# Performance work log

Measured on AMD Instinct MI355X. Metric: run time of the kernel, lower is better.

The kernel has to match this reference:

```python
import jax, jax.numpy as jnp
import numpy as np

NEG_INF = -1e9


def setup_inputs() -> dict:
    key = jax.random.key(0)
    k1, k2, k3 = jax.random.split(key, 3)
    B, C, Q, D = 64, 1024, 128, 128
    context = jax.random.normal(k1, (B, C, D), dtype=jnp.float32)
    query = jax.random.normal(k2, (B, Q, D), dtype=jnp.float32)
    W = jax.random.normal(k3, (3 * D, 1), dtype=jnp.float32)
    query_mask = jnp.ones((B, Q), dtype=jnp.float32)
    return {"context": context, "query": query, "W": W, "query_mask": query_mask}


def reference(context, query, W, query_mask):
    # Dense(1) over concat([c, q, c*q]) decomposes as c.w_c + q.w_q + (c*w_s).q
    D = context.shape[-1]
    w = W[:, 0]
    w_c, w_q, w_s = w[:D], w[D:2 * D], w[2 * D:]
    c_term = jnp.einsum('bcd,d->bc', context, w_c)          # [B,C]
    q_term = jnp.einsum('bqd,d->bq', query, w_q)            # [B,Q]
    s_term = jnp.einsum('bcd,bqd->bcq', context * w_s, query)  # [B,C,Q]
    S = c_term[:, :, None] + q_term[:, None, :] + s_term    # [B,C,Q]
    S = S + (1.0 - query_mask)[:, None, :] * NEG_INF
    c2q_scores = jax.nn.softmax(S, axis=2)                  # [B,C,Q]
    c2q = jnp.einsum('bcq,bqd->bcd', c2q_scores, query)     # [B,C,D]
    q2c_scores = jax.nn.softmax(jnp.max(S, axis=2), axis=1)  # [B,C]
    q2c = jnp.einsum('bc,bcd->bd', q2c_scores, context)     # [B,D]
    q2c = q2c[:, None, :]                                   # broadcast over C
    out = jnp.concatenate([context, c2q, context * c2q, context * q2c], axis=-1)
    return out
```

## Files before the change

### kernel.cpp

```cpp
#include <hip/hip_runtime.h>

#define NEGINF -1000000000.0f

typedef __attribute__((ext_vector_type(4))) float f32x4;
typedef _Float16 half8 __attribute__((ext_vector_type(8)));
typedef _Float16 half4 __attribute__((ext_vector_type(4)));

constexpr int Bn = 64, Cn = 1024, Qn = 128, Dn = 128;
constexpr int QSTR = 144;
constexpr int CSTR = 132;


__global__ __launch_bounds__(256) void k1_kernel(
    const float* __restrict__ ctx, const float* __restrict__ qry,
    const float* __restrict__ W, const float* __restrict__ mask,
    float* __restrict__ out, float* __restrict__ ws_part, float* __restrict__ ws_ms)
{
    __shared__ char smem[77376];
    _Float16* qrow = (_Float16*)smem;
    _Float16* qT2  = (_Float16*)(smem + 36864);
    float* wfull = (float*)(smem + 73728);
    float* qts   = (float*)(smem + 75264);
    float* cts   = (float*)(smem + 75776);
    float* mloc  = (float*)(smem + 76288);
    float* wv    = (float*)(smem + 76800);
    float* red   = (float*)(smem + 77312);
    float* partf = (float*)(smem + 36864);
    float* cq    = (float*)smem;

    const int b = blockIdx.y, cg = blockIdx.x, c0 = cg * 128;
    const int t = threadIdx.x;
    const float* ctxB = ctx + (size_t)b * Cn * Dn;
    const float* qryB = qry + (size_t)b * Qn * Dn;

    for (int i = t; i < 384; i += 256) wfull[i] = W[i];
    __syncthreads();

    {
        int q = t >> 1, h = t & 1;
        const float* qr = qryB + q * Dn + h * 64;
        int p = ((q >> 5) << 5) + 8 * ((q >> 2) & 3) + (q & 3) + 4 * ((q >> 4) & 1);
        float acc = 0.f;
        for (int j = 0; j < 64; j += 4) {
            f32x4 v = *(const f32x4*)(qr + j);
            int d = h * 64 + j;
            acc += v.x * wfull[128 + d] + v.y * wfull[128 + d + 1]
                 + v.z * wfull[128 + d + 2] + v.w * wfull[128 + d + 3];
            half4 hv;
            hv[0] = (_Float16)v.x; hv[1] = (_Float16)v.y;
            hv[2] = (_Float16)v.z; hv[3] = (_Float16)v.w;
            *(half4*)&qrow[q * QSTR + d] = hv;
            qT2[(d + 0) * QSTR + p] = hv[0];
            qT2[(d + 1) * QSTR + p] = hv[1];
            qT2[(d + 2) * QSTR + p] = hv[2];
            qT2[(d + 3) * QSTR + p] = hv[3];
        }
        acc += __shfl_xor(acc, 1);
        if (h == 0) qts[q] = acc + (1.0f - mask[b * Qn + q]) * NEGINF;
    }
    {
        int c = t >> 1, h = t & 1;
        const float* cr = ctxB + (size_t)(c0 + c) * Dn + h * 64;
        float acc = 0.f;
        for (int j = 0; j < 64; j += 4) {
            f32x4 v = *(const f32x4*)(cr + j);
            int d = h * 64 + j;
            acc += v.x * wfull[d] + v.y * wfull[d + 1] + v.z * wfull[d + 2] + v.w * wfull[d + 3];
        }
        acc += __shfl_xor(acc, 1);
        if (h == 0) cts[c] = acc;
    }
    __syncthreads();

    const int wave = t >> 6, lane = t & 63, g = lane >> 4, l15 = lane & 15;
    const int cw = wave * 32;

    f32x4 acc1[8][2] = {};
#pragma unroll
    for (int kk = 0; kk < 4; ++kk) {
        const int dbase = kk * 32 + g * 8;
        f32x4 w0 = *(const f32x4*)&wfull[256 + dbase];
        f32x4 w1 = *(const f32x4*)&wfull[256 + dbase + 4];
        half8 ah[2], al[2];
#pragma unroll
        for (int nt = 0; nt < 2; ++nt) {
            const float* p = ctxB + (size_t)(c0 + cw + nt * 16 + l15) * Dn + dbase;
            f32x4 v0 = *(const f32x4*)p, v1 = *(const f32x4*)(p + 4);
            float av[8] = {v0.x * w0.x, v0.y * w0.y, v0.z * w0.z, v0.w * w0.w,
                           v1.x * w1.x, v1.y * w1.y, v1.z * w1.z, v1.w * w1.w};
#pragma unroll
            for (int j = 0; j < 8; ++j) {
                _Float16 hh = (_Float16)av[j];
                ah[nt][j] = hh;
                al[nt][j] = (_Float16)(av[j] - (float)hh);
            }
        }
#pragma unroll
        for (int mt = 0; mt < 8; ++mt) {
            half8 qf = *(const half8*)&qrow[(mt * 16 + l15) * QSTR + dbase];
#pragma unroll
            for (int nt = 0; nt < 2; ++nt) {
                acc1[mt][nt] = __builtin_amdgcn_mfma_f32_16x16x32_f16(qf, ah[nt], acc1[mt][nt], 0, 0, 0);
                acc1[mt][nt] = __builtin_amdgcn_mfma_f32_16x16x32_f16(qf, al[nt], acc1[mt][nt], 0, 0, 0);
            }
        }
    }

#pragma unroll
    for (int mt = 0; mt < 8; ++mt)
#pragma unroll
        for (int r = 0; r < 4; ++r) {
            float qv = qts[mt * 16 + g * 4 + r];
            acc1[mt][0][r] += qv;
            acc1[mt][1][r] += qv;
        }

    float psum[2];
#pragma unroll
    for (int nt = 0; nt < 2; ++nt) {
        float mx = -3.4e38f;
#pragma unroll
        for (int mt = 0; mt < 8; ++mt)
#pragma unroll
            for (int r = 0; r < 4; ++r) mx = fmaxf(mx, acc1[mt][nt][r]);
        mx = fmaxf(mx, __shfl_xor(mx, 16));
        mx = fmaxf(mx, __shfl_xor(mx, 32));
        float sum = 0.f;
#pragma unroll
        for (int mt = 0; mt < 8; ++mt)
#pragma unroll
            for (int r = 0; r < 4; ++r) {
                float pv = __expf(acc1[mt][nt][r] - mx);
                acc1[mt][nt][r] = pv;
                sum += pv;
            }
        sum += __shfl_xor(sum, 16);
        sum += __shfl_xor(sum, 32);
        psum[nt] = sum;
        int cl = cw + nt * 16 + l15;
        if (g == 0) mloc[cl] = mx + cts[cl];
    }

    half8 pa[4][2];
#pragma unroll
    for (int kk2 = 0; kk2 < 4; ++kk2)
#pragma unroll
        for (int nt = 0; nt < 2; ++nt)
#pragma unroll
            for (int j = 0; j < 8; ++j)
                pa[kk2][nt][j] = (_Float16)acc1[2 * kk2 + (j >> 2)][nt][j & 3];

    float inv[2][4];
#pragma unroll
    for (int nt = 0; nt < 2; ++nt)
#pragma unroll
        for (int r = 0; r < 4; ++r)
            inv[nt][r] = 1.0f / __shfl(psum[nt], g * 4 + r);

    f32x4 acc2[2][8] = {};
#pragma unroll
    for (int kk2 = 0; kk2 < 4; ++kk2)
#pragma unroll
        for (int ntD = 0; ntD < 8; ++ntD) {
            half8 qb = *(const half8*)&qT2[(ntD * 16 + l15) * QSTR + kk2 * 32 + 8 * g];
#pragma unroll
            for (int nt1 = 0; nt1 < 2; ++nt1)
                acc2[nt1][ntD] = __builtin_amdgcn_mfma_f32_16x16x32_f16(pa[kk2][nt1], qb, acc2[nt1][ntD], 0, 0, 0);
        }
    __syncthreads();

    float Mloc;
    {
        float v = (t < 128) ? mloc[t] : -3.4e38f;
        float m = v;
#pragma unroll
        for (int off = 1; off < 64; off <<= 1) m = fmaxf(m, __shfl_xor(m, off));
        if (lane == 0) red[wave] = m;
        __syncthreads();
        Mloc = fmaxf(fmaxf(red[0], red[1]), fmaxf(red[2], red[3]));
        float e = (t < 128) ? __expf(v - Mloc) : 0.f;
        if (t < 128) wv[t] = e;
        float s = e;
#pragma unroll
        for (int off = 1; off < 64; off <<= 1) s += __shfl_xor(s, off);
        if (lane == 0) red[4 + wave] = s;
        __syncthreads();
    }
    float Sloc = red[4] + red[5] + red[6] + red[7];
    {
        int grp = t >> 5, d4 = (t & 31) * 4;
        const float* cb = ctxB + (size_t)(c0 + grp * 16) * Dn;
        f32x4 a = {};
        for (int i = 0; i < 16; ++i) {
            f32x4 cv = *(const f32x4*)(cb + (size_t)i * Dn + d4);
            float w = wv[grp * 16 + i];
            a.x += w * cv.x; a.y += w * cv.y; a.z += w * cv.z; a.w += w * cv.w;
        }
        *(f32x4*)&partf[grp * 128 + d4] = a;
        __syncthreads();
        if (t < 128) {
            float s = 0.f;
#pragma unroll
            for (int g2 = 0; g2 < 8; ++g2) s += partf[g2 * 128 + t];
            ws_part[((size_t)(b * 8 + cg)) * 128 + t] = s;
        }
        if (t == 0) {
            ws_ms[(b * 8 + cg) * 2 + 0] = Mloc;
            ws_ms[(b * 8 + cg) * 2 + 1] = Sloc;
        }
    }
    __syncthreads();

#pragma unroll
    for (int nt1 = 0; nt1 < 2; ++nt1)
#pragma unroll
        for (int r = 0; r < 4; ++r) {
            int c = cw + nt1 * 16 + g * 4 + r;
            float is = inv[nt1][r];
#pragma unroll
            for (int ntD = 0; ntD < 8; ++ntD)
                cq[c * CSTR + ntD * 16 + l15] = acc2[nt1][ntD][r] * is;
        }
    __syncthreads();
    for (int step = 0; step < 16; ++step) {
        int c = (t >> 5) + step * 8, d4 = (t & 31) * 4;
        f32x4 q = *(const f32x4*)&cq[c * CSTR + d4];
        f32x4 cv = *(const f32x4*)(ctxB + (size_t)(c0 + c) * Dn + d4);
        float* orow = out + ((size_t)(b * Cn + c0 + c)) * 512;
        *(f32x4*)(orow + 128 + d4) = q;
        f32x4 pr;
        pr.x = cv.x * q.x; pr.y = cv.y * q.y; pr.z = cv.z * q.z; pr.w = cv.w * q.w;
        *(f32x4*)(orow + 256 + d4) = pr;
    }
}

__global__ __launch_bounds__(256) void k3_kernel(
    const float* __restrict__ ctx, const float* __restrict__ ws_part,
    const float* __restrict__ ws_ms, float* __restrict__ out)
{
    __shared__ float q2cs[128];
    const int ct = blockIdx.x, b = blockIdx.y, t = threadIdx.x;
    if (t < 128) {
        const float* ms = ws_ms + b * 16;
        float Mg = -3.4e38f;
#pragma unroll
        for (int i = 0; i < 8; ++i) Mg = fmaxf(Mg, ms[2 * i]);
        float num = 0.f, den = 0.f;
#pragma unroll
        for (int i = 0; i < 8; ++i) {
            float e = __expf(ms[2 * i] - Mg);
            num += e * ws_part[((size_t)(b * 8 + i)) * 128 + t];
            den += e * ms[2 * i + 1];
        }
        q2cs[t] = num / den;
    }
    __syncthreads();
    const float* cb = ctx + ((size_t)b * Cn + ct * 128) * Dn;
    float* ob = out + ((size_t)(b * Cn) + ct * 128) * 512;
    for (int step = 0; step < 16; ++step) {
        int c = (t >> 5) + step * 8, d4 = (t & 31) * 4;
        f32x4 v = *(const f32x4*)(cb + (size_t)c * Dn + d4);
        f32x4 q = *(const f32x4*)&q2cs[d4];
        *(f32x4*)(ob + (size_t)c * 512 + d4) = v;
        f32x4 w;
        w.x = v.x * q.x; w.y = v.y * q.y; w.z = v.z * q.z; w.w = v.w * q.w;
        *(f32x4*)(ob + (size_t)c * 512 + 384 + d4) = w;
    }
}

extern "C" void kernel_launch(void* const* d_in, const int* in_sizes, int n_in,
                              void* d_out, int out_size, void* d_ws, size_t ws_size,
                              hipStream_t stream) {
    const float* ctx  = (const float*)d_in[0];
    const float* qry  = (const float*)d_in[1];
    const float* W    = (const float*)d_in[2];
    const float* mask = (const float*)d_in[3];
    float* out = (float*)d_out;

    float* ws_part = (float*)d_ws;
    float* ws_ms   = ws_part + (size_t)Bn * 8 * 128;

    k1_kernel<<<dim3(8, Bn), 256, 0, stream>>>(ctx, qry, W, mask, out, ws_part, ws_ms);
    k3_kernel<<<dim3(8, Bn), 256, 0, stream>>>(ctx, ws_part, ws_ms, out);
}
```

Baseline: 55.71 us.

## Fuse q2c pass into main kernel with per-batch atomic grid sync

Merges the second kernel into the first: each block publishes its partial q2c sums with atomic stores, bumps a per-batch counter, then spin-waits until all eight blocks of its batch have arrived before computing q2c and writing all four output slices. Context rows are kept in registers so they are not read from global memory again. A small reset kernel zeroes the counters, shared memory is shrunk (QSTR reduced) and launch bounds request two blocks per CU so that co-residency makes the spin-wait safe. The risks are deadlock if the blocks of one batch are not co-resident, higher register pressure from the cached context rows, and a serialized wait on the slowest block.

Measured after the change: 104.9 us. 88.3% more time.

```diff
diff --git a/kernel.cpp b/kernel.cpp
--- a/kernel.cpp
+++ b/kernel.cpp
@@ -7,25 +7,31 @@
 typedef _Float16 half4 __attribute__((ext_vector_type(4)));
 
 constexpr int Bn = 64, Cn = 1024, Qn = 128, Dn = 128;
-constexpr int QSTR = 144;
+constexpr int QSTR = 136;
 constexpr int CSTR = 132;
 
 
-__global__ __launch_bounds__(256) void k1_kernel(
+__global__ void reset_kernel(unsigned* __restrict__ cnt) {
+    cnt[threadIdx.x] = 0u;
+}
+
+__global__ __launch_bounds__(256, 2) void fused_kernel(
     const float* __restrict__ ctx, const float* __restrict__ qry,
     const float* __restrict__ W, const float* __restrict__ mask,
-    float* __restrict__ out, float* __restrict__ ws_part, float* __restrict__ ws_ms)
+    float* __restrict__ out, float* __restrict__ ws_part,
+    float* __restrict__ ws_ms, unsigned* __restrict__ cnt)
 {
-    __shared__ char smem[77376];
+    __shared__ char smem[73792];
     _Float16* qrow = (_Float16*)smem;
-    _Float16* qT2  = (_Float16*)(smem + 36864);
-    float* wfull = (float*)(smem + 73728);
-    float* qts   = (float*)(smem + 75264);
-    float* cts   = (float*)(smem + 75776);
-    float* mloc  = (float*)(smem + 76288);
-    float* wv    = (float*)(smem + 76800);
-    float* red   = (float*)(smem + 77312);
-    float* partf = (float*)(smem + 36864);
+    _Float16* qT2  = (_Float16*)(smem + 34816);
+    float* wfull = (float*)(smem + 69632);
+    float* qts   = (float*)(smem + 71168);
+    float* cts   = (float*)(smem + 71680);
+    float* mloc  = (float*)(smem + 72192);
+    float* wv    = (float*)(smem + 72704);
+    float* red   = (float*)(smem + 73216);
+    float* q2cs  = (float*)(smem + 73280);
+    float* partf = (float*)(smem + 34816);
     float* cq    = (float*)smem;
 
     const int b = blockIdx.y, cg = blockIdx.x, c0 = cg * 128;
@@ -187,14 +193,18 @@
         __syncthreads();
     }
     float Sloc = red[4] + red[5] + red[6] + red[7];
-    {
-        int grp = t >> 5, d4 = (t & 31) * 4;
+
+    const int grp = t >> 5, d4 = (t & 31) * 4;
+    f32x4 cvr[16];
+    {
         const float* cb = ctxB + (size_t)(c0 + grp * 16) * Dn;
         f32x4 a = {};
+#pragma unroll
         for (int i = 0; i < 16; ++i) {
-            f32x4 cv = *(const f32x4*)(cb + (size_t)i * Dn + d4);
+            cvr[i] = *(const f32x4*)(cb + (size_t)i * Dn + d4);
             float w = wv[grp * 16 + i];
-            a.x += w * cv.x; a.y += w * cv.y; a.z += w * cv.z; a.w += w * cv.w;
+            a.x += w * cvr[i].x; a.y += w * cvr[i].y;
+            a.z += w * cvr[i].z; a.w += w * cvr[i].w;
         }
         *(f32x4*)&partf[grp * 128 + d4] = a;
         __syncthreads();
@@ -202,14 +212,21 @@
             float s = 0.f;
 #pragma unroll
             for (int g2 = 0; g2 < 8; ++g2) s += partf[g2 * 128 + t];
-            ws_part[((size_t)(b * 8 + cg)) * 128 + t] = s;
+            __hip_atomic_store(&ws_part[((size_t)(b * 8 + cg)) * 128 + t], s,
+                               __ATOMIC_RELAXED, __HIP_MEMORY_SCOPE_AGENT);
         }
         if (t == 0) {
-            ws_ms[(b * 8 + cg) * 2 + 0] = Mloc;
-            ws_ms[(b * 8 + cg) * 2 + 1] = Sloc;
-        }
-    }
-    __syncthreads();
+            __hip_atomic_store(&ws_ms[(b * 8 + cg) * 2 + 0], Mloc,
+                               __ATOMIC_RELAXED, __HIP_MEMORY_SCOPE_AGENT);
+            __hip_atomic_store(&ws_ms[(b * 8 + cg) * 2 + 1], Sloc,
+                               __ATOMIC_RELAXED, __HIP_MEMORY_SCOPE_AGENT);
+        }
+    }
+    __syncthreads();
+    if (t == 0) {
+        __threadfence();
+        __hip_atomic_fetch_add(&cnt[b], 1u, __ATOMIC_RELEASE, __HIP_MEMORY_SCOPE_AGENT);
+    }
 
 #pragma unroll
     for (int nt1 = 0; nt1 < 2; ++nt1)
@@ -221,50 +238,49 @@
             for (int ntD = 0; ntD < 8; ++ntD)
                 cq[c * CSTR + ntD * 16 + l15] = acc2[nt1][ntD][r] * is;
         }
-    __syncthreads();
-    for (int step = 0; step < 16; ++step) {
-        int c = (t >> 5) + step * 8, d4 = (t & 31) * 4;
-        f32x4 q = *(const f32x4*)&cq[c * CSTR + d4];
-        f32x4 cv = *(const f32x4*)(ctxB + (size_t)(c0 + c) * Dn + d4);
-        float* orow = out + ((size_t)(b * Cn + c0 + c)) * 512;
-        *(f32x4*)(orow + 128 + d4) = q;
-        f32x4 pr;
-        pr.x = cv.x * q.x; pr.y = cv.y * q.y; pr.z = cv.z * q.z; pr.w = cv.w * q.w;
-        *(f32x4*)(orow + 256 + d4) = pr;
-    }
-}
-
-__global__ __launch_bounds__(256) void k3_kernel(
-    const float* __restrict__ ctx, const float* __restrict__ ws_part,
-    const float* __restrict__ ws_ms, float* __restrict__ out)
-{
-    __shared__ float q2cs[128];
-    const int ct = blockIdx.x, b = blockIdx.y, t = threadIdx.x;
+
+    if (t == 0) {
+        while (__hip_atomic_load(&cnt[b], __ATOMIC_ACQUIRE, __HIP_MEMORY_SCOPE_AGENT) < 8u)
+            __builtin_amdgcn_s_sleep(2);
+        __threadfence();
+    }
+    __syncthreads();
     if (t < 128) {
-        const float* ms = ws_ms + b * 16;
         float Mg = -3.4e38f;
-#pragma unroll
-        for (int i = 0; i < 8; ++i) Mg = fmaxf(Mg, ms[2 * i]);
+        float msv[16];
+#pragma unroll
+        for (int i = 0; i < 16; ++i)
+            msv[i] = __hip_atomic_load(&ws_ms[b * 16 + i], __ATOMIC_RELAXED, __HIP_MEMORY_SCOPE_AGENT);
+#pragma unroll
+        for (int i = 0; i < 8; ++i) Mg = fmaxf(Mg, msv[2 * i]);
         float num = 0.f, den = 0.f;
 #pragma unroll
         for (int i = 0; i < 8; ++i) {
-            float e = __expf(ms[2 * i] - Mg);
-            num += e * ws_part[((size_t)(b * 8 + i)) * 128 + t];
-            den += e * ms[2 * i + 1];
+            float e = __expf(msv[2 * i] - Mg);
+            num += e * __hip_atomic_load(&ws_part[((size_t)(b * 8 + i)) * 128 + t],
+                                         __ATOMIC_RELAXED, __HIP_MEMORY_SCOPE_AGENT);
+            den += e * msv[2 * i + 1];
         }
         q2cs[t] = num / den;
     }
     __syncthreads();
-    const float* cb = ctx + ((size_t)b * Cn + ct * 128) * Dn;
-    float* ob = out + ((size_t)(b * Cn) + ct * 128) * 512;
-    for (int step = 0; step < 16; ++step) {
-        int c = (t >> 5) + step * 8, d4 = (t & 31) * 4;
-        f32x4 v = *(const f32x4*)(cb + (size_t)c * Dn + d4);
-        f32x4 q = *(const f32x4*)&q2cs[d4];
-        *(f32x4*)(ob + (size_t)c * 512 + d4) = v;
-        f32x4 w;
-        w.x = v.x * q.x; w.y = v.y * q.y; w.z = v.z * q.z; w.w = v.w * q.w;
-        *(f32x4*)(ob + (size_t)c * 512 + 384 + d4) = w;
+
+    {
+        f32x4 qv = *(const f32x4*)&q2cs[d4];
+#pragma unroll
+        for (int i = 0; i < 16; ++i) {
+            int c = grp * 16 + i;
+            f32x4 cv = cvr[i];
+            f32x4 cqv = *(const f32x4*)&cq[c * CSTR + d4];
+            float* orow = out + ((size_t)(b * Cn + c0 + c)) * 512;
+            *(f32x4*)(orow + d4) = cv;
+            *(f32x4*)(orow + 128 + d4) = cqv;
+            f32x4 p2, p3;
+            p2.x = cv.x * cqv.x; p2.y = cv.y * cqv.y; p2.z = cv.z * cqv.z; p2.w = cv.w * cqv.w;
+            p3.x = cv.x * qv.x;  p3.y = cv.y * qv.y;  p3.z = cv.z * qv.z;  p3.w = cv.w * qv.w;
+            *(f32x4*)(orow + 256 + d4) = p2;
+            *(f32x4*)(orow + 384 + d4) = p3;
+        }
     }
 }
 
@@ -279,7 +295,8 @@
 
     float* ws_part = (float*)d_ws;
     float* ws_ms   = ws_part + (size_t)Bn * 8 * 128;
-
-    k1_kernel<<<dim3(8, Bn), 256, 0, stream>>>(ctx, qry, W, mask, out, ws_part, ws_ms);
-    k3_kernel<<<dim3(8, Bn), 256, 0, stream>>>(ctx, ws_part, ws_ms, out);
+    unsigned* cnt  = (unsigned*)(ws_ms + (size_t)Bn * 16);
+
+    reset_kernel<<<dim3(1), 64, 0, stream>>>(cnt);
+    fused_kernel<<<dim3(8, Bn), 256, 0, stream>>>(ctx, qry, W, mask, out, ws_part, ws_ms, cnt);
 }
```

## Double k1 block to 512 threads, one 16-row C tile per wave

Applied to the files above, without the earlier changes.

The first kernel now runs 512 threads (8 waves) per block, each wave owning 16 context rows instead of 32. This halves per-thread accumulator registers and doubles waves per block to improve latency hiding. The context-weight dot product is folded into the MFMA operand load loop, removing a separate pass over context, and the Q smem stride shrinks from 144 to 136 to cut LDS use. The smaller stride may change LDS bank-conflict behaviour, and the extra waves add synchronisation cost.

Result: faster. 51.48 us (-7.6%).

```diff
diff --git a/kernel.cpp b/kernel.cpp
--- a/kernel.cpp
+++ b/kernel.cpp
@@ -7,25 +7,24 @@
 typedef _Float16 half4 __attribute__((ext_vector_type(4)));
 
 constexpr int Bn = 64, Cn = 1024, Qn = 128, Dn = 128;
-constexpr int QSTR = 144;
+constexpr int QSTR = 136;
 constexpr int CSTR = 132;
 
 
-__global__ __launch_bounds__(256) void k1_kernel(
+__global__ __launch_bounds__(512, 4) void k1_kernel(
     const float* __restrict__ ctx, const float* __restrict__ qry,
     const float* __restrict__ W, const float* __restrict__ mask,
     float* __restrict__ out, float* __restrict__ ws_part, float* __restrict__ ws_ms)
 {
-    __shared__ char smem[77376];
+    __shared__ char smem[72768];
     _Float16* qrow = (_Float16*)smem;
-    _Float16* qT2  = (_Float16*)(smem + 36864);
-    float* wfull = (float*)(smem + 73728);
-    float* qts   = (float*)(smem + 75264);
-    float* cts   = (float*)(smem + 75776);
-    float* mloc  = (float*)(smem + 76288);
-    float* wv    = (float*)(smem + 76800);
-    float* red   = (float*)(smem + 77312);
-    float* partf = (float*)(smem + 36864);
+    _Float16* qT2  = (_Float16*)(smem + 34816);
+    float* wfull = (float*)(smem + 69632);
+    float* qts   = (float*)(smem + 71168);
+    float* mloc  = (float*)(smem + 71680);
+    float* wv    = (float*)(smem + 72192);
+    float* red   = (float*)(smem + 72704);
+    float* partf = (float*)(smem + 34816);
     float* cq    = (float*)smem;
 
     const int b = blockIdx.y, cg = blockIdx.x, c0 = cg * 128;
@@ -33,17 +32,17 @@
     const float* ctxB = ctx + (size_t)b * Cn * Dn;
     const float* qryB = qry + (size_t)b * Qn * Dn;
 
-    for (int i = t; i < 384; i += 256) wfull[i] = W[i];
+    if (t < 384) wfull[t] = W[t];
     __syncthreads();
 
     {
-        int q = t >> 1, h = t & 1;
-        const float* qr = qryB + q * Dn + h * 64;
+        int q = t >> 2, h = t & 3;
+        const float* qr = qryB + q * Dn + h * 32;
         int p = ((q >> 5) << 5) + 8 * ((q >> 2) & 3) + (q & 3) + 4 * ((q >> 4) & 1);
         float acc = 0.f;
-        for (int j = 0; j < 64; j += 4) {
+        for (int j = 0; j < 32; j += 4) {
             f32x4 v = *(const f32x4*)(qr + j);
-            int d = h * 64 + j;
+            int d = h * 32 + j;
             acc += v.x * wfull[128 + d] + v.y * wfull[128 + d + 1]
                  + v.z * wfull[128 + d + 2] + v.w * wfull[128 + d + 3];
             half4 hv;
@@ -56,174 +55,147 @@
             qT2[(d + 3) * QSTR + p] = hv[3];
         }
         acc += __shfl_xor(acc, 1);
+        acc += __shfl_xor(acc, 2);
         if (h == 0) qts[q] = acc + (1.0f - mask[b * Qn + q]) * NEGINF;
     }
-    {
-        int c = t >> 1, h = t & 1;
-        const float* cr = ctxB + (size_t)(c0 + c) * Dn + h * 64;
-        float acc = 0.f;
-        for (int j = 0; j < 64; j += 4) {
-            f32x4 v = *(const f32x4*)(cr + j);
-            int d = h * 64 + j;
-            acc += v.x * wfull[d] + v.y * wfull[d + 1] + v.z * wfull[d + 2] + v.w * wfull[d + 3];
-        }
-        acc += __shfl_xor(acc, 1);
-        if (h == 0) cts[c] = acc;
-    }
     __syncthreads();
 
     const int wave = t >> 6, lane = t & 63, g = lane >> 4, l15 = lane & 15;
-    const int cw = wave * 32;
-
-    f32x4 acc1[8][2] = {};
+    const int cw = wave * 16;
+    const int cl = cw + l15;
+
+    f32x4 acc1[8] = {};
+    float cterm = 0.f;
 #pragma unroll
     for (int kk = 0; kk < 4; ++kk) {
         const int dbase = kk * 32 + g * 8;
-        f32x4 w0 = *(const f32x4*)&wfull[256 + dbase];
-        f32x4 w1 = *(const f32x4*)&wfull[256 + dbase + 4];
-        half8 ah[2], al[2];
-#pragma unroll
-        for (int nt = 0; nt < 2; ++nt) {
-            const float* p = ctxB + (size_t)(c0 + cw + nt * 16 + l15) * Dn + dbase;
-            f32x4 v0 = *(const f32x4*)p, v1 = *(const f32x4*)(p + 4);
-            float av[8] = {v0.x * w0.x, v0.y * w0.y, v0.z * w0.z, v0.w * w0.w,
-                           v1.x * w1.x, v1.y * w1.y, v1.z * w1.z, v1.w * w1.w};
-#pragma unroll
-            for (int j = 0; j < 8; ++j) {
-                _Float16 hh = (_Float16)av[j];
-                ah[nt][j] = hh;
-                al[nt][j] = (_Float16)(av[j] - (float)hh);
-            }
+        const float* pc = ctxB + (size_t)(c0 + cl) * Dn + dbase;
+        f32x4 v0 = *(const f32x4*)pc, v1 = *(const f32x4*)(pc + 4);
+        f32x4 s0 = *(const f32x4*)&wfull[256 + dbase], s1 = *(const f32x4*)&wfull[256 + dbase + 4];
+        f32x4 c0w = *(const f32x4*)&wfull[dbase], c1w = *(const f32x4*)&wfull[dbase + 4];
+        cterm += v0.x * c0w.x + v0.y * c0w.y + v0.z * c0w.z + v0.w * c0w.w
+               + v1.x * c1w.x + v1.y * c1w.y + v1.z * c1w.z + v1.w * c1w.w;
+        float av[8] = {v0.x * s0.x, v0.y * s0.y, v0.z * s0.z, v0.w * s0.w,
+                       v1.x * s1.x, v1.y * s1.y, v1.z * s1.z, v1.w * s1.w};
+        half8 ah, al;
+#pragma unroll
+        for (int j = 0; j < 8; ++j) {
+            _Float16 hh = (_Float16)av[j];
+            ah[j] = hh;
+            al[j] = (_Float16)(av[j] - (float)hh);
         }
 #pragma unroll
         for (int mt = 0; mt < 8; ++mt) {
             half8 qf = *(const half8*)&qrow[(mt * 16 + l15) * QSTR + dbase];
-#pragma unroll
-            for (int nt = 0; nt < 2; ++nt) {
-                acc1[mt][nt] = __builtin_amdgcn_mfma_f32_16x16x32_f16(qf, ah[nt], acc1[mt][nt], 0, 0, 0);
-                acc1[mt][nt] = __builtin_amdgcn_mfma_f32_16x16x32_f16(qf, al[nt], acc1[mt][nt], 0, 0, 0);
-            }
-        }
-    }
+            acc1[mt] = __builtin_amdgcn_mfma_f32_16x16x32_f16(qf, ah, acc1[mt], 0, 0, 0);
+            acc1[mt] = __builtin_amdgcn_mfma_f32_16x16x32_f16(qf, al, acc1[mt], 0, 0, 0);
+        }
+    }
+    cterm += __shfl_xor(cterm, 16);
+    cterm += __shfl_xor(cterm, 32);
 
 #pragma unroll
     for (int mt = 0; mt < 8; ++mt)
 #pragma unroll
+        for (int r = 0; r < 4; ++r) acc1[mt][r] += qts[mt * 16 + g * 4 + r];
+
+    float mx = -3.4e38f;
+#pragma unroll
+    for (int mt = 0; mt < 8; ++mt)
+#pragma unroll
+        for (int r = 0; r < 4; ++r) mx = fmaxf(mx, acc1[mt][r]);
+    mx = fmaxf(mx, __shfl_xor(mx, 16));
+    mx = fmaxf(mx, __shfl_xor(mx, 32));
+    float sum = 0.f;
+#pragma unroll
+    for (int mt = 0; mt < 8; ++mt)
+#pragma unroll
         for (int r = 0; r < 4; ++r) {
-            float qv = qts[mt * 16 + g * 4 + r];
-            acc1[mt][0][r] += qv;
-            acc1[mt][1][r] += qv;
-        }
-
-    float psum[2];
-#pragma unroll
-    for (int nt = 0; nt < 2; ++nt) {
-        float mx = -3.4e38f;
-#pragma unroll
-        for (int mt = 0; mt < 8; ++mt)
-#pragma unroll
-            for (int r = 0; r < 4; ++r) mx = fmaxf(mx, acc1[mt][nt][r]);
-        mx = fmaxf(mx, __shfl_xor(mx, 16));
-        mx = fmaxf(mx, __shfl_xor(mx, 32));
-        float sum = 0.f;
-#pragma unroll
-        for (int mt = 0; mt < 8; ++mt)
-#pragma unroll
-            for (int r = 0; r < 4; ++r) {
-                float pv = __expf(acc1[mt][nt][r] - mx);
-                acc1[mt][nt][r] = pv;
-                sum += pv;
-            }
-        sum += __shfl_xor(sum, 16);
-        sum += __shfl_xor(sum, 32);
-        psum[nt] = sum;
-        int cl = cw + nt * 16 + l15;
-        if (g == 0) mloc[cl] = mx + cts[cl];
-    }
-
-    half8 pa[4][2];
+            float pv = __expf(acc1[mt][r] - mx);
+            acc1[mt][r] = pv;
+            sum += pv;
+        }
+    sum += __shfl_xor(sum, 16);
+    sum += __shfl_xor(sum, 32);
+    if (g == 0) mloc[cl] = mx + cterm;
+
+    half8 pa[4];
 #pragma unroll
     for (int kk2 = 0; kk2 < 4; ++kk2)
 #pragma unroll
-        for (int nt = 0; nt < 2; ++nt)
-#pragma unroll
-            for (int j = 0; j < 8; ++j)
-                pa[kk2][nt][j] = (_Float16)acc1[2 * kk2 + (j >> 2)][nt][j & 3];
-
-    float inv[2][4];
-#pragma unroll
-    for (int nt = 0; nt < 2; ++nt)
-#pragma unroll
-        for (int r = 0; r < 4; ++r)
-            inv[nt][r] = 1.0f / __shfl(psum[nt], g * 4 + r);
-
-    f32x4 acc2[2][8] = {};
+        for (int j = 0; j < 8; ++j)
+            pa[kk2][j] = (_Float16)acc1[2 * kk2 + (j >> 2)][j & 3];
+
+    float inv[4];
+#pragma unroll
+    for (int r = 0; r < 4; ++r) inv[r] = 1.0f / __shfl(sum, g * 4 + r);
+
+    f32x4 acc2[8] = {};
 #pragma unroll
     for (int kk2 = 0; kk2 < 4; ++kk2)
 #pragma unroll
         for (int ntD = 0; ntD < 8; ++ntD) {
             half8 qb = *(const half8*)&qT2[(ntD * 16 + l15) * QSTR + kk2 * 32 + 8 * g];
-#pragma unroll
-            for (int nt1 = 0; nt1 < 2; ++nt1)
-                acc2[nt1][ntD] = __builtin_amdgcn_mfma_f32_16x16x32_f16(pa[kk2][nt1], qb, acc2[nt1][ntD], 0, 0, 0);
-        }
-    __syncthreads();
-
-    float Mloc;
+            acc2[ntD] = __builtin_amdgcn_mfma_f32_16x16x32_f16(pa[kk2], qb, acc2[ntD], 0, 0, 0);
+        }
+    __syncthreads();
+
+    float vm = mloc[t & 127];
+    float m = vm;
+#pragma unroll
+    for (int off = 1; off < 64; off <<= 1) m = fmaxf(m, __shfl_xor(m, off));
+    if (lane == 0) red[wave] = m;
+    __syncthreads();
+    float Mloc = red[0];
+#pragma unroll
+    for (int i = 1; i < 8; ++i) Mloc = fmaxf(Mloc, red[i]);
+    float e = __expf(vm - Mloc);
+    if (t < 128) wv[t] = e;
+    float s = e;
+#pragma unroll
+    for (int off = 1; off < 64; off <<= 1) s += __shfl_xor(s, off);
+    if (lane == 0) red[8 + wave] = s;
+    __syncthreads();
+    float Sloc = red[8] + red[9];
+
+    const int grp = t >> 5, d4 = (t & 31) * 4;
     {
-        float v = (t < 128) ? mloc[t] : -3.4e38f;
-        float m = v;
-#pragma unroll
-        for (int off = 1; off < 64; off <<= 1) m = fmaxf(m, __shfl_xor(m, off));
-        if (lane == 0) red[wave] = m;
-        __syncthreads();
-        Mloc = fmaxf(fmaxf(red[0], red[1]), fmaxf(red[2], red[3]));
-        float e = (t < 128) ? __expf(v - Mloc) : 0.f;
-        if (t < 128) wv[t] = e;
-        float s = e;
-#pragma unroll
-        for (int off = 1; off < 64; off <<= 1) s += __shfl_xor(s, off);
-        if (lane == 0) red[4 + wave] = s;
-        __syncthreads();
-    }
-    float Sloc = red[4] + red[5] + red[6] + red[7];
-    {
-        int grp = t >> 5, d4 = (t & 31) * 4;
-        const float* cb = ctxB + (size_t)(c0 + grp * 16) * Dn;
+        const float* cb = ctxB + (size_t)(c0 + grp * 8) * Dn;
         f32x4 a = {};
-        for (int i = 0; i < 16; ++i) {
+#pragma unroll
+        for (int i = 0; i < 8; ++i) {
             f32x4 cv = *(const f32x4*)(cb + (size_t)i * Dn + d4);
-            float w = wv[grp * 16 + i];
+            float w = wv[grp * 8 + i];
             a.x += w * cv.x; a.y += w * cv.y; a.z += w * cv.z; a.w += w * cv.w;
         }
         *(f32x4*)&partf[grp * 128 + d4] = a;
-        __syncthreads();
-        if (t < 128) {
-            float s = 0.f;
-#pragma unroll
-            for (int g2 = 0; g2 < 8; ++g2) s += partf[g2 * 128 + t];
-            ws_part[((size_t)(b * 8 + cg)) * 128 + t] = s;
-        }
-        if (t == 0) {
-            ws_ms[(b * 8 + cg) * 2 + 0] = Mloc;
-            ws_ms[(b * 8 + cg) * 2 + 1] = Sloc;
-        }
-    }
-    __syncthreads();
-
-#pragma unroll
-    for (int nt1 = 0; nt1 < 2; ++nt1)
-#pragma unroll
-        for (int r = 0; r < 4; ++r) {
-            int c = cw + nt1 * 16 + g * 4 + r;
-            float is = inv[nt1][r];
-#pragma unroll
-            for (int ntD = 0; ntD < 8; ++ntD)
-                cq[c * CSTR + ntD * 16 + l15] = acc2[nt1][ntD][r] * is;
-        }
-    __syncthreads();
-    for (int step = 0; step < 16; ++step) {
-        int c = (t >> 5) + step * 8, d4 = (t & 31) * 4;
+    }
+    __syncthreads();
+    if (t < 128) {
+        float s2 = 0.f;
+#pragma unroll
+        for (int g2 = 0; g2 < 16; ++g2) s2 += partf[g2 * 128 + t];
+        ws_part[((size_t)(b * 8 + cg)) * 128 + t] = s2;
+    }
+    if (t == 0) {
+        ws_ms[(b * 8 + cg) * 2 + 0] = Mloc;
+        ws_ms[(b * 8 + cg) * 2 + 1] = Sloc;
+    }
+    __syncthreads();
+
+#pragma unroll
+    for (int r = 0; r < 4; ++r) {
+        int c = cw + g * 4 + r;
+        float is = inv[r];
+#pragma unroll
+        for (int ntD = 0; ntD < 8; ++ntD)
+            cq[c * CSTR + ntD * 16 + l15] = acc2[ntD][r] * is;
+    }
+    __syncthreads();
+
+#pragma unroll
+    for (int step = 0; step < 8; ++step) {
+        int c = grp + step * 16;
         f32x4 q = *(const f32x4*)&cq[c * CSTR + d4];
         f32x4 cv = *(const f32x4*)(ctxB + (size_t)(c0 + c) * Dn + d4);
         float* orow = out + ((size_t)(b * Cn + c0 + c)) * 512;
@@ -280,6 +252,6 @@
     float* ws_part = (float*)d_ws;
     float* ws_ms   = ws_part + (size_t)Bn * 8 * 128;
 
-    k1_kernel<<<dim3(8, Bn), 256, 0, stream>>>(ctx, qry, W, mask, out, ws_part, ws_ms);
+    k1_kernel<<<dim3(8, Bn), 512, 0, stream>>>(ctx, qry, W, mask, out, ws_part, ws_ms);
     k3_kernel<<<dim3(8, Bn), 256, 0, stream>>>(ctx, ws_part, ws_ms, out);
 }
```
